# Performance work log

Measured on AMD Instinct MI355X. Metric: run time of the kernel, lower is better.

The kernel has to match this reference:

```python
import jax, jax.numpy as jnp
import numpy as np

ENSEMBLE_MAX_MEAN = 0.5  # weight on max-pooled similarity
EPS = 1e-12


def _l2norm(x, axis):
    return x / jnp.sqrt(jnp.sum(x * x, axis=axis, keepdims=True) + EPS)


def setup_inputs() -> dict:
    key = jax.random.key(0)
    k1, k2 = jax.random.split(key)
    image_feat = jax.random.normal(k1, (8, 512, 32, 32), dtype=jnp.float32)  # [B,C,H,W]
    proto_emb = jax.random.normal(k2, (150, 32, 512), dtype=jnp.float32)    # [N,K,C]
    return {"image_feat": image_feat, "proto_emb": proto_emb}


def reference(image_feat, proto_emb):
    # cosine similarity branch of FreeDAMasker.forward_seg
    # image_feat: [B,C,H,W], proto_emb: [N,K,C]
    img = _l2norm(image_feat, axis=1)
    pro = _l2norm(proto_emb, axis=-1)
    # simmap: [B,N,K,H,W]
    simmap = jnp.einsum('bchw,nkc->bnkhw', img, pro)
    sim_max = jnp.max(simmap, axis=2)   # [B,N,H,W]
    sim_mean = jnp.mean(simmap, axis=2)  # [B,N,H,W]
    sim = ENSEMBLE_MAX_MEAN * sim_max + (1.0 - ENSEMBLE_MAX_MEAN) * sim_mean
    # sim2mask: deterministic=True, hard=False -> soft sigmoid mask
    soft_mask = jax.nn.sigmoid(sim)
    return soft_mask, sim
```

## Files before the change

kernel.cpp:

```cpp
#include <hip/hip_runtime.h>
#include <hip/hip_bf16.h>

#define NPROT 150
#define KPROT 32
#define CDIM  512
#define BDIM  8
#define HWDIM 1024
#define MDIM  (NPROT * KPROT)
#define PDIM  (BDIM * HWDIM)

typedef int   i32x4 __attribute__((ext_vector_type(4)));

#define QSCALE 508.0f
#define DEQ2   ((0.25f / 127.0f) * (0.25f / 127.0f))

__device__ __forceinline__ unsigned short f2bf(float x) {
  unsigned int u = __float_as_uint(x);
  u = u + 0x7fffu + ((u >> 16) & 1u);
  return (unsigned short)(u >> 16);
}
__device__ __forceinline__ float bf2f(unsigned short s) {
  return __uint_as_float(((unsigned int)s) << 16);
}
__device__ __forceinline__ int q8(float x) {
  float v = fminf(fmaxf(x * QSCALE, -127.0f), 127.0f);
  return __float2int_rn(v);
}
__device__ __forceinline__ unsigned int pack4(int a, int b, int c, int d) {
  return (unsigned int)((a & 255) | ((b & 255) << 8) | ((c & 255) << 16) | ((d & 255) << 24));
}

#define GLOAD_LDS16(gsrc, ldst) __builtin_amdgcn_global_load_lds(            \
    (const __attribute__((address_space(1))) void*)(gsrc),                   \
    (__attribute__((address_space(3))) void*)(ldst), 16, 0, 0)

__global__ __launch_bounds__(256) void prep_k(const float* __restrict__ img,
                                              const float* __restrict__ proto,
                                              char* __restrict__ Ai8,
                                              char* __restrict__ Bi8) {
  __shared__ unsigned short tile[32][520];
  __shared__ float partial[8][32];
  __shared__ float invn[32];
  int t   = threadIdx.x;
  int bid = blockIdx.x;
  if (bid >= 256) {
    int row  = (bid - 256) * 4 + (t >> 6);
    int lane = t & 63;
    const float4* rp = (const float4*)(proto + (size_t)row * CDIM);
    float4 v0 = rp[lane * 2];
    float4 v1 = rp[lane * 2 + 1];
    float ss = v0.x*v0.x + v0.y*v0.y + v0.z*v0.z + v0.w*v0.w
             + v1.x*v1.x + v1.y*v1.y + v1.z*v1.z + v1.w*v1.w;
    #pragma unroll
    for (int o = 32; o > 0; o >>= 1) ss += __shfl_xor(ss, o, 64);
    float inv = rsqrtf(ss + 1e-12f);
    uint2 o8;
    o8.x = pack4(q8(v0.x*inv), q8(v0.y*inv), q8(v0.z*inv), q8(v0.w*inv));
    o8.y = pack4(q8(v1.x*inv), q8(v1.y*inv), q8(v1.z*inv), q8(v1.w*inv));
    *(uint2*)(Ai8 + (size_t)row * CDIM + lane * 8) = o8;
    return;
  }
  int b   = bid >> 5;
  int hw0 = (bid & 31) << 5;
  int hwo = t & 31;
  int cg  = t >> 5;
  const float* base = img + ((size_t)b << 19) + hw0 + hwo;
  float ss = 0.f;
  #pragma unroll 8
  for (int i = 0; i < 64; ++i) {
    int c = i * 8 + cg;
    float v = base[(size_t)c << 10];
    ss += v * v;
    tile[hwo][c] = f2bf(v);
  }
  partial[cg][hwo] = ss;
  __syncthreads();
  if (t < 32) {
    float s = 0.f;
    #pragma unroll
    for (int j = 0; j < 8; ++j) s += partial[j][t];
    invn[t] = rsqrtf(s + 1e-12f);
  }
  __syncthreads();
  int r  = t >> 3;
  int c0 = (t & 7) * 64;
  float sc = invn[r];
  char* dst = Bi8 + ((((size_t)b << 10) + hw0 + r)) * CDIM + c0;
  #pragma unroll
  for (int j = 0; j < 8; ++j) {
    float x0 = bf2f(tile[r][c0 + j*8 + 0]) * sc;
    float x1 = bf2f(tile[r][c0 + j*8 + 1]) * sc;
    float x2 = bf2f(tile[r][c0 + j*8 + 2]) * sc;
    float x3 = bf2f(tile[r][c0 + j*8 + 3]) * sc;
    float x4 = bf2f(tile[r][c0 + j*8 + 4]) * sc;
    float x5 = bf2f(tile[r][c0 + j*8 + 5]) * sc;
    float x6 = bf2f(tile[r][c0 + j*8 + 6]) * sc;
    float x7 = bf2f(tile[r][c0 + j*8 + 7]) * sc;
    uint2 o8;
    o8.x = pack4(q8(x0), q8(x1), q8(x2), q8(x3));
    o8.y = pack4(q8(x4), q8(x5), q8(x6), q8(x7));
    *(uint2*)(dst + j * 8) = o8;
  }
}

__global__ __launch_bounds__(256, 3) void gemm_k(const char* __restrict__ Ai8,
                                                 const char* __restrict__ Bi8,
                                                 float* __restrict__ out) {
  __shared__ __align__(16) char smem[(64 + 256) * 128];
  char* As = smem;
  char* Bs = smem + 64 * 128;

  int t    = threadIdx.x;
  int lane = t & 63;
  int w    = t >> 6;
  int lr   = lane & 15;
  int lg   = lane >> 4;
  int m0   = blockIdx.y * 64;
  int p0   = blockIdx.x * 256;

  i32x4 acc[4][4] = {};

  const char* Ab = Ai8 + (size_t)m0 * CDIM;
  const char* Bb = Bi8 + (size_t)p0 * CDIM;

  for (int c0 = 0; c0 < CDIM; c0 += 128) {
    #pragma unroll
    for (int it = 0; it < 2; ++it) {
      int gi  = it * 256 + t;
      int row = gi >> 3, g = gi & 7;
      int gs  = g ^ (row & 7);
      GLOAD_LDS16(Ab + (size_t)row * CDIM + c0 + gs * 16, As + gi * 16);
    }
    #pragma unroll
    for (int it = 0; it < 8; ++it) {
      int gi  = it * 256 + t;
      int row = gi >> 3, g = gi & 7;
      int gs  = g ^ (row & 7);
      GLOAD_LDS16(Bb + (size_t)row * CDIM + c0 + gs * 16, Bs + gi * 16);
    }
    __syncthreads();

    #pragma unroll
    for (int ks = 0; ks < 2; ++ks) {
      int gbase = ks * 4 + lg;
      i32x4 a4[4], b4[4];
      #pragma unroll
      for (int f = 0; f < 4; ++f) {
        int row = f * 16 + lr;
        a4[f] = *(const i32x4*)(As + row * 128 + (gbase ^ (row & 7)) * 16);
      }
      #pragma unroll
      for (int f = 0; f < 4; ++f) {
        int row = w * 64 + f * 16 + lr;
        b4[f] = *(const i32x4*)(Bs + row * 128 + (gbase ^ (row & 7)) * 16);
      }
      #pragma unroll
      for (int fm = 0; fm < 4; ++fm)
        #pragma unroll
        for (int fp = 0; fp < 4; ++fp)
          acc[fm][fp] = __builtin_amdgcn_mfma_i32_16x16x64_i8(a4[fm], b4[fp], acc[fm][fp], 0, 0, 0);
    }
    __syncthreads();
  }

  #pragma unroll
  for (int gi2 = 0; gi2 < 2; ++gi2) {
    #pragma unroll
    for (int fp = 0; fp < 4; ++fp) {
      float mx = -1e30f, sm = 0.f;
      #pragma unroll
      for (int fm = 2 * gi2; fm < 2 * gi2 + 2; ++fm)
        #pragma unroll
        for (int r = 0; r < 4; ++r) {
          float v = (float)acc[fm][fp][r] * DEQ2;
          mx = fmaxf(mx, v);
          sm += v;
        }
      mx = fmaxf(mx, __shfl_xor(mx, 16, 64));
      mx = fmaxf(mx, __shfl_xor(mx, 32, 64));
      sm += __shfl_xor(sm, 16, 64);
      sm += __shfl_xor(sm, 32, 64);
      if (lg == 0) {
        float sim  = 0.5f * mx + sm * (0.5f / 32.0f);
        float mask = 1.0f / (1.0f + __expf(-sim));
        int n  = blockIdx.y * 2 + gi2;
        int p  = p0 + w * 64 + fp * 16 + lr;
        int b  = p >> 10, hw = p & 1023;
        size_t o = ((size_t)(b * NPROT + n) << 10) + hw;
        out[o] = mask;
        out[(size_t)(BDIM * NPROT * HWDIM) + o] = sim;
      }
    }
  }
}

extern "C" void kernel_launch(void* const* d_in, const int* in_sizes, int n_in,
                              void* d_out, int out_size, void* d_ws, size_t ws_size,
                              hipStream_t stream) {
  const float* img   = (const float*)d_in[0];
  const float* proto = (const float*)d_in[1];
  float* out = (float*)d_out;
  char* Ai8 = (char*)d_ws;
  char* Bi8 = Ai8 + (size_t)MDIM * CDIM;

  prep_k<<<256 + MDIM / 4, 256, 0, stream>>>(img, proto, Ai8, Bi8);
  gemm_k<<<dim3(PDIM / 256, MDIM / 64), 256, 0, stream>>>(Ai8, Bi8, out);
}
```

Baseline: 45.04 us.

## Double-buffer int8 GEMM stages and quantize raw image features with deferred norm

```diff
diff --git a/kernel.cpp b/kernel.cpp
--- a/kernel.cpp
+++ b/kernel.cpp
@@ -9,22 +9,17 @@
 #define MDIM  (NPROT * KPROT)
 #define PDIM  (BDIM * HWDIM)
 
-typedef int   i32x4 __attribute__((ext_vector_type(4)));
-
-#define QSCALE 508.0f
-#define DEQ2   ((0.25f / 127.0f) * (0.25f / 127.0f))
-
-__device__ __forceinline__ unsigned short f2bf(float x) {
-  unsigned int u = __float_as_uint(x);
-  u = u + 0x7fffu + ((u >> 16) & 1u);
-  return (unsigned short)(u >> 16);
-}
-__device__ __forceinline__ float bf2f(unsigned short s) {
-  return __uint_as_float(((unsigned int)s) << 16);
-}
-__device__ __forceinline__ int q8(float x) {
-  float v = fminf(fmaxf(x * QSCALE, -127.0f), 127.0f);
-  return __float2int_rn(v);
+typedef int i32x4 __attribute__((ext_vector_type(4)));
+
+#define QSA 508.0f
+#define QSB 24.0f
+#define DEQAB (1.0f / (508.0f * 24.0f))
+
+__device__ __forceinline__ int q8a(float x) {
+  return __float2int_rn(fminf(fmaxf(x * QSA, -127.0f), 127.0f));
+}
+__device__ __forceinline__ int q8b(float x) {
+  return __float2int_rn(fminf(fmaxf(x * QSB, -127.0f), 127.0f));
 }
 __device__ __forceinline__ unsigned int pack4(int a, int b, int c, int d) {
   return (unsigned int)((a & 255) | ((b & 255) << 8) | ((c & 255) << 16) | ((d & 255) << 24));
@@ -37,10 +32,10 @@
 __global__ __launch_bounds__(256) void prep_k(const float* __restrict__ img,
                                               const float* __restrict__ proto,
                                               char* __restrict__ Ai8,
-                                              char* __restrict__ Bi8) {
-  __shared__ unsigned short tile[32][520];
-  __shared__ float partial[8][32];
-  __shared__ float invn[32];
+                                              char* __restrict__ Bi8,
+                                              float* __restrict__ invB) {
+  __shared__ char tile[32][528];
+  __shared__ float psum[8][32];
   int t   = threadIdx.x;
   int bid = blockIdx.x;
   if (bid >= 256) {
@@ -55,8 +50,8 @@
     for (int o = 32; o > 0; o >>= 1) ss += __shfl_xor(ss, o, 64);
     float inv = rsqrtf(ss + 1e-12f);
     uint2 o8;
-    o8.x = pack4(q8(v0.x*inv), q8(v0.y*inv), q8(v0.z*inv), q8(v0.w*inv));
-    o8.y = pack4(q8(v1.x*inv), q8(v1.y*inv), q8(v1.z*inv), q8(v1.w*inv));
+    o8.x = pack4(q8a(v0.x*inv), q8a(v0.y*inv), q8a(v0.z*inv), q8a(v0.w*inv));
+    o8.y = pack4(q8a(v1.x*inv), q8a(v1.y*inv), q8a(v1.z*inv), q8a(v1.w*inv));
     *(uint2*)(Ai8 + (size_t)row * CDIM + lane * 8) = o8;
     return;
   }
@@ -66,49 +61,40 @@
   int cg  = t >> 5;
   const float* base = img + ((size_t)b << 19) + hw0 + hwo;
   float ss = 0.f;
-  #pragma unroll 8
-  for (int i = 0; i < 64; ++i) {
-    int c = i * 8 + cg;
-    float v = base[(size_t)c << 10];
-    ss += v * v;
-    tile[hwo][c] = f2bf(v);
-  }
-  partial[cg][hwo] = ss;
+  #pragma unroll 4
+  for (int i = 0; i < 64; i += 4) {
+    int c = cg * 64 + i;
+    float x0 = base[(size_t)(c + 0) << 10];
+    float x1 = base[(size_t)(c + 1) << 10];
+    float x2 = base[(size_t)(c + 2) << 10];
+    float x3 = base[(size_t)(c + 3) << 10];
+    ss += x0*x0 + x1*x1 + x2*x2 + x3*x3;
+    *(unsigned int*)&tile[hwo][c] = pack4(q8b(x0), q8b(x1), q8b(x2), q8b(x3));
+  }
+  psum[cg][hwo] = ss;
   __syncthreads();
   if (t < 32) {
     float s = 0.f;
     #pragma unroll
-    for (int j = 0; j < 8; ++j) s += partial[j][t];
-    invn[t] = rsqrtf(s + 1e-12f);
-  }
-  __syncthreads();
-  int r  = t >> 3;
-  int c0 = (t & 7) * 64;
-  float sc = invn[r];
-  char* dst = Bi8 + ((((size_t)b << 10) + hw0 + r)) * CDIM + c0;
+    for (int j = 0; j < 8; ++j) s += psum[j][t];
+    invB[((size_t)b << 10) + hw0 + t] = rsqrtf(s + 1e-12f);
+  }
   #pragma unroll
-  for (int j = 0; j < 8; ++j) {
-    float x0 = bf2f(tile[r][c0 + j*8 + 0]) * sc;
-    float x1 = bf2f(tile[r][c0 + j*8 + 1]) * sc;
-    float x2 = bf2f(tile[r][c0 + j*8 + 2]) * sc;
-    float x3 = bf2f(tile[r][c0 + j*8 + 3]) * sc;
-    float x4 = bf2f(tile[r][c0 + j*8 + 4]) * sc;
-    float x5 = bf2f(tile[r][c0 + j*8 + 5]) * sc;
-    float x6 = bf2f(tile[r][c0 + j*8 + 6]) * sc;
-    float x7 = bf2f(tile[r][c0 + j*8 + 7]) * sc;
-    uint2 o8;
-    o8.x = pack4(q8(x0), q8(x1), q8(x2), q8(x3));
-    o8.y = pack4(q8(x4), q8(x5), q8(x6), q8(x7));
-    *(uint2*)(dst + j * 8) = o8;
-  }
-}
-
-__global__ __launch_bounds__(256, 3) void gemm_k(const char* __restrict__ Ai8,
+  for (int it = 0; it < 4; ++it) {
+    int gi  = it * 256 + t;
+    int pix = gi >> 5, gr = gi & 31;
+    int4 v = *(const int4*)&tile[pix][gr * 16];
+    *(int4*)(Bi8 + (((size_t)b << 10) + hw0 + pix) * CDIM + gr * 16) = v;
+  }
+}
+
+__global__ __launch_bounds__(256, 2) void gemm_k(const char* __restrict__ Ai8,
                                                  const char* __restrict__ Bi8,
+                                                 const float* __restrict__ invB,
                                                  float* __restrict__ out) {
-  __shared__ __align__(16) char smem[(64 + 256) * 128];
+  __shared__ __align__(16) char smem[81920];
   char* As = smem;
-  char* Bs = smem + 64 * 128;
+  char* Bs = smem + 16384;
 
   int t    = threadIdx.x;
   int lane = t & 63;
@@ -123,45 +109,65 @@
   const char* Ab = Ai8 + (size_t)m0 * CDIM;
   const char* Bb = Bi8 + (size_t)p0 * CDIM;
 
-  for (int c0 = 0; c0 < CDIM; c0 += 128) {
-    #pragma unroll
-    for (int it = 0; it < 2; ++it) {
-      int gi  = it * 256 + t;
-      int row = gi >> 3, g = gi & 7;
-      int gs  = g ^ (row & 7);
-      GLOAD_LDS16(Ab + (size_t)row * CDIM + c0 + gs * 16, As + gi * 16);
-    }
-    #pragma unroll
-    for (int it = 0; it < 8; ++it) {
-      int gi  = it * 256 + t;
-      int row = gi >> 3, g = gi & 7;
-      int gs  = g ^ (row & 7);
-      GLOAD_LDS16(Bb + (size_t)row * CDIM + c0 + gs * 16, Bs + gi * 16);
-    }
-    __syncthreads();
-
-    #pragma unroll
-    for (int ks = 0; ks < 2; ++ks) {
-      int gbase = ks * 4 + lg;
-      i32x4 a4[4], b4[4];
-      #pragma unroll
-      for (int f = 0; f < 4; ++f) {
-        int row = f * 16 + lr;
-        a4[f] = *(const i32x4*)(As + row * 128 + (gbase ^ (row & 7)) * 16);
-      }
-      #pragma unroll
-      for (int f = 0; f < 4; ++f) {
-        int row = w * 64 + f * 16 + lr;
-        b4[f] = *(const i32x4*)(Bs + row * 128 + (gbase ^ (row & 7)) * 16);
-      }
-      #pragma unroll
-      for (int fm = 0; fm < 4; ++fm)
-        #pragma unroll
-        for (int fp = 0; fp < 4; ++fp)
-          acc[fm][fp] = __builtin_amdgcn_mfma_i32_16x16x64_i8(a4[fm], b4[fp], acc[fm][fp], 0, 0, 0);
-    }
-    __syncthreads();
-  }
+#define STAGE(S) do {                                                         \
+    const int buf_ = (S) & 1; const int cb_ = (S) * 128;                      \
+    _Pragma("unroll")                                                         \
+    for (int it = 0; it < 2; ++it) {                                          \
+      int gi = it * 256 + t, row = gi >> 3, g = gi & 7;                       \
+      int gs = g ^ (row & 7);                                                 \
+      GLOAD_LDS16(Ab + (size_t)row * CDIM + cb_ + gs * 16,                    \
+                  As + buf_ * 8192 + gi * 16);                                \
+    }                                                                         \
+    _Pragma("unroll")                                                         \
+    for (int it = 0; it < 8; ++it) {                                          \
+      int gi = it * 256 + t, row = gi >> 3, g = gi & 7;                       \
+      int gs = g ^ (row & 7);                                                 \
+      GLOAD_LDS16(Bb + (size_t)row * CDIM + cb_ + gs * 16,                    \
+                  Bs + buf_ * 32768 + gi * 16);                               \
+    }                                                                         \
+    __builtin_amdgcn_sched_barrier(0);                                        \
+  } while (0)
+
+#define WAITV0() { asm volatile("s_waitcnt vmcnt(0)" ::: "memory");           \
+                   __builtin_amdgcn_sched_barrier(0); }
+#define BAR() { __builtin_amdgcn_sched_barrier(0);                            \
+                __builtin_amdgcn_s_barrier();                                 \
+                __builtin_amdgcn_sched_barrier(0); }
+
+#define COMPUTE(S) do {                                                       \
+    const char* Ap_ = As + ((S) & 1) * 8192;                                  \
+    const char* Bp_ = Bs + ((S) & 1) * 32768;                                 \
+    _Pragma("unroll")                                                         \
+    for (int ks = 0; ks < 2; ++ks) {                                          \
+      int gb_ = ks * 4 + lg;                                                  \
+      i32x4 a4[4], b4[4];                                                     \
+      _Pragma("unroll")                                                       \
+      for (int f = 0; f < 4; ++f) {                                           \
+        int row = f * 16 + lr;                                                \
+        a4[f] = *(const i32x4*)(Ap_ + row * 128 + (gb_ ^ (row & 7)) * 16);    \
+      }                                                                       \
+      _Pragma("unroll")                                                       \
+      for (int f = 0; f < 4; ++f) {                                           \
+        int row = w * 64 + f * 16 + lr;                                       \
+        b4[f] = *(const i32x4*)(Bp_ + row * 128 + (gb_ ^ (row & 7)) * 16);    \
+      }                                                                       \
+      __builtin_amdgcn_s_setprio(1);                                          \
+      _Pragma("unroll")                                                       \
+      for (int fm = 0; fm < 4; ++fm)                                          \
+        _Pragma("unroll")                                                     \
+        for (int fp = 0; fp < 4; ++fp)                                        \
+          acc[fm][fp] = __builtin_amdgcn_mfma_i32_16x16x64_i8(                \
+              a4[fm], b4[fp], acc[fm][fp], 0, 0, 0);                          \
+      __builtin_amdgcn_s_setprio(0);                                          \
+    }                                                                         \
+  } while (0)
+
+  STAGE(0);
+  WAITV0(); BAR();
+  STAGE(1); COMPUTE(0); WAITV0(); BAR();
+  STAGE(2); COMPUTE(1); WAITV0(); BAR();
+  STAGE(3); COMPUTE(2); WAITV0(); BAR();
+  COMPUTE(3);
 
   #pragma unroll
   for (int gi2 = 0; gi2 < 2; ++gi2) {
@@ -172,7 +178,7 @@
       for (int fm = 2 * gi2; fm < 2 * gi2 + 2; ++fm)
         #pragma unroll
         for (int r = 0; r < 4; ++r) {
-          float v = (float)acc[fm][fp][r] * DEQ2;
+          float v = (float)acc[fm][fp][r];
           mx = fmaxf(mx, v);
           sm += v;
         }
@@ -181,10 +187,11 @@
       sm += __shfl_xor(sm, 16, 64);
       sm += __shfl_xor(sm, 32, 64);
       if (lg == 0) {
-        float sim  = 0.5f * mx + sm * (0.5f / 32.0f);
-        float mask = 1.0f / (1.0f + __expf(-sim));
+        int p  = p0 + w * 64 + fp * 16 + lr;
+        float scale = DEQAB * invB[p];
+        float sim   = (0.5f * mx + sm * (0.5f / 32.0f)) * scale;
+        float mask  = 1.0f / (1.0f + __expf(-sim));
         int n  = blockIdx.y * 2 + gi2;
-        int p  = p0 + w * 64 + fp * 16 + lr;
         int b  = p >> 10, hw = p & 1023;
         size_t o = ((size_t)(b * NPROT + n) << 10) + hw;
         out[o] = mask;
@@ -192,6 +199,10 @@
       }
     }
   }
+#undef STAGE
+#undef WAITV0
+#undef BAR
+#undef COMPUTE
 }
 
 extern "C" void kernel_launch(void* const* d_in, const int* in_sizes, int n_in,
@@ -200,9 +211,10 @@
   const float* img   = (const float*)d_in[0];
   const float* proto = (const float*)d_in[1];
   float* out = (float*)d_out;
-  char* Ai8 = (char*)d_ws;
-  char* Bi8 = Ai8 + (size_t)MDIM * CDIM;
-
-  prep_k<<<256 + MDIM / 4, 256, 0, stream>>>(img, proto, Ai8, Bi8);
-  gemm_k<<<dim3(PDIM / 256, MDIM / 64), 256, 0, stream>>>(Ai8, Bi8, out);
-}
+  char*  Ai8  = (char*)d_ws;
+  char*  Bi8  = Ai8 + (size_t)MDIM * CDIM;
+  float* invB = (float*)(Bi8 + (size_t)PDIM * CDIM);
+
+  prep_k<<<256 + MDIM / 4, 256, 0, stream>>>(img, proto, Ai8, Bi8, invB);
+  gemm_k<<<dim3(PDIM / 256, MDIM / 64), 256, 0, stream>>>(Ai8, Bi8, invB, out);
+}
```

Measured after the change: 48.26 us. +7.1%, slower.

## Quantize raw image features directly and defer L2 normalization to GEMM epilogue

Applied to the files above, without the earlier changes.

```diff
diff --git a/kernel.cpp b/kernel.cpp
--- a/kernel.cpp
+++ b/kernel.cpp
@@ -9,22 +9,17 @@
 #define MDIM  (NPROT * KPROT)
 #define PDIM  (BDIM * HWDIM)
 
-typedef int   i32x4 __attribute__((ext_vector_type(4)));
+typedef int i32x4 __attribute__((ext_vector_type(4)));
 
-#define QSCALE 508.0f
-#define DEQ2   ((0.25f / 127.0f) * (0.25f / 127.0f))
+#define QSA 508.0f
+#define QSB 24.0f
+#define DEQAB (1.0f / (508.0f * 24.0f))
 
-__device__ __forceinline__ unsigned short f2bf(float x) {
-  unsigned int u = __float_as_uint(x);
-  u = u + 0x7fffu + ((u >> 16) & 1u);
-  return (unsigned short)(u >> 16);
+__device__ __forceinline__ int q8a(float x) {
+  return __float2int_rn(fminf(fmaxf(x * QSA, -127.0f), 127.0f));
 }
-__device__ __forceinline__ float bf2f(unsigned short s) {
-  return __uint_as_float(((unsigned int)s) << 16);
-}
-__device__ __forceinline__ int q8(float x) {
-  float v = fminf(fmaxf(x * QSCALE, -127.0f), 127.0f);
-  return __float2int_rn(v);
+__device__ __forceinline__ int q8b(float x) {
+  return __float2int_rn(fminf(fmaxf(x * QSB, -127.0f), 127.0f));
 }
 __device__ __forceinline__ unsigned int pack4(int a, int b, int c, int d) {
   return (unsigned int)((a & 255) | ((b & 255) << 8) | ((c & 255) << 16) | ((d & 255) << 24));
@@ -37,10 +32,10 @@
 __global__ __launch_bounds__(256) void prep_k(const float* __restrict__ img,
                                               const float* __restrict__ proto,
                                               char* __restrict__ Ai8,
-                                              char* __restrict__ Bi8) {
-  __shared__ unsigned short tile[32][520];
-  __shared__ float partial[8][32];
-  __shared__ float invn[32];
+                                              char* __restrict__ Bi8,
+                                              float* __restrict__ invB) {
+  __shared__ char tile[32][528];
+  __shared__ float psum[8][32];
   int t   = threadIdx.x;
   int bid = blockIdx.x;
   if (bid >= 256) {
@@ -55,8 +50,8 @@
     for (int o = 32; o > 0; o >>= 1) ss += __shfl_xor(ss, o, 64);
     float inv = rsqrtf(ss + 1e-12f);
     uint2 o8;
-    o8.x = pack4(q8(v0.x*inv), q8(v0.y*inv), q8(v0.z*inv), q8(v0.w*inv));
-    o8.y = pack4(q8(v1.x*inv), q8(v1.y*inv), q8(v1.z*inv), q8(v1.w*inv));
+    o8.x = pack4(q8a(v0.x*inv), q8a(v0.y*inv), q8a(v0.z*inv), q8a(v0.w*inv));
+    o8.y = pack4(q8a(v1.x*inv), q8a(v1.y*inv), q8a(v1.z*inv), q8a(v1.w*inv));
     *(uint2*)(Ai8 + (size_t)row * CDIM + lane * 8) = o8;
     return;
   }
@@ -66,45 +61,36 @@
   int cg  = t >> 5;
   const float* base = img + ((size_t)b << 19) + hw0 + hwo;
   float ss = 0.f;
-  #pragma unroll 8
-  for (int i = 0; i < 64; ++i) {
-    int c = i * 8 + cg;
-    float v = base[(size_t)c << 10];
-    ss += v * v;
-    tile[hwo][c] = f2bf(v);
+  #pragma unroll 4
+  for (int i = 0; i < 64; i += 4) {
+    int c = cg * 64 + i;
+    float x0 = base[(size_t)(c + 0) << 10];
+    float x1 = base[(size_t)(c + 1) << 10];
+    float x2 = base[(size_t)(c + 2) << 10];
+    float x3 = base[(size_t)(c + 3) << 10];
+    ss += x0*x0 + x1*x1 + x2*x2 + x3*x3;
+    *(unsigned int*)&tile[hwo][c] = pack4(q8b(x0), q8b(x1), q8b(x2), q8b(x3));
   }
-  partial[cg][hwo] = ss;
+  psum[cg][hwo] = ss;
   __syncthreads();
   if (t < 32) {
     float s = 0.f;
     #pragma unroll
-    for (int j = 0; j < 8; ++j) s += partial[j][t];
-    invn[t] = rsqrtf(s + 1e-12f);
+    for (int j = 0; j < 8; ++j) s += psum[j][t];
+    invB[((size_t)b << 10) + hw0 + t] = rsqrtf(s + 1e-12f);
   }
-  __syncthreads();
-  int r  = t >> 3;
-  int c0 = (t & 7) * 64;
-  float sc = invn[r];
-  char* dst = Bi8 + ((((size_t)b << 10) + hw0 + r)) * CDIM + c0;
   #pragma unroll
-  for (int j = 0; j < 8; ++j) {
-    float x0 = bf2f(tile[r][c0 + j*8 + 0]) * sc;
-    float x1 = bf2f(tile[r][c0 + j*8 + 1]) * sc;
-    float x2 = bf2f(tile[r][c0 + j*8 + 2]) * sc;
-    float x3 = bf2f(tile[r][c0 + j*8 + 3]) * sc;
-    float x4 = bf2f(tile[r][c0 + j*8 + 4]) * sc;
-    float x5 = bf2f(tile[r][c0 + j*8 + 5]) * sc;
-    float x6 = bf2f(tile[r][c0 + j*8 + 6]) * sc;
-    float x7 = bf2f(tile[r][c0 + j*8 + 7]) * sc;
-    uint2 o8;
-    o8.x = pack4(q8(x0), q8(x1), q8(x2), q8(x3));
-    o8.y = pack4(q8(x4), q8(x5), q8(x6), q8(x7));
-    *(uint2*)(dst + j * 8) = o8;
+  for (int it = 0; it < 4; ++it) {
+    int gi  = it * 256 + t;
+    int pix = gi >> 5, gr = gi & 31;
+    int4 v = *(const int4*)&tile[pix][gr * 16];
+    *(int4*)(Bi8 + (((size_t)b << 10) + hw0 + pix) * CDIM + gr * 16) = v;
   }
 }
 
-__global__ __launch_bounds__(256, 3) void gemm_k(const char* __restrict__ Ai8,
+__global__ __launch_bounds__(256, 4) void gemm_k(const char* __restrict__ Ai8,
                                                  const char* __restrict__ Bi8,
+                                                 const float* __restrict__ invB,
                                                  float* __restrict__ out) {
   __shared__ __align__(16) char smem[(64 + 256) * 128];
   char* As = smem;
@@ -172,7 +158,7 @@
       for (int fm = 2 * gi2; fm < 2 * gi2 + 2; ++fm)
         #pragma unroll
         for (int r = 0; r < 4; ++r) {
-          float v = (float)acc[fm][fp][r] * DEQ2;
+          float v = (float)acc[fm][fp][r];
           mx = fmaxf(mx, v);
           sm += v;
         }
@@ -181,10 +167,11 @@
       sm += __shfl_xor(sm, 16, 64);
       sm += __shfl_xor(sm, 32, 64);
       if (lg == 0) {
-        float sim  = 0.5f * mx + sm * (0.5f / 32.0f);
-        float mask = 1.0f / (1.0f + __expf(-sim));
+        int p  = p0 + w * 64 + fp * 16 + lr;
+        float scale = DEQAB * invB[p];
+        float sim   = (0.5f * mx + sm * (0.5f / 32.0f)) * scale;
+        float mask  = 1.0f / (1.0f + __expf(-sim));
         int n  = blockIdx.y * 2 + gi2;
-        int p  = p0 + w * 64 + fp * 16 + lr;
         int b  = p >> 10, hw = p & 1023;
         size_t o = ((size_t)(b * NPROT + n) << 10) + hw;
         out[o] = mask;
@@ -200,9 +187,10 @@
   const float* img   = (const float*)d_in[0];
   const float* proto = (const float*)d_in[1];
   float* out = (float*)d_out;
-  char* Ai8 = (char*)d_ws;
-  char* Bi8 = Ai8 + (size_t)MDIM * CDIM;
+  char*  Ai8  = (char*)d_ws;
+  char*  Bi8  = Ai8 + (size_t)MDIM * CDIM;
+  float* invB = (float*)(Bi8 + (size_t)PDIM * CDIM);
 
-  prep_k<<<256 + MDIM / 4, 256, 0, stream>>>(img, proto, Ai8, Bi8);
-  gemm_k<<<dim3(PDIM / 256, MDIM / 64), 256, 0, stream>>>(Ai8, Bi8, out);
+  prep_k<<<256 + MDIM / 4, 256, 0, stream>>>(img, proto, Ai8, Bi8, invB);
+  gemm_k<<<dim3(PDIM / 256, MDIM / 64), 256, 0, stream>>>(Ai8, Bi8, invB, out);
 }
```

Measured after the change: 41.99 us. 6.8% less time.
